# Performance work log

Hardware: AMD Instinct MI355X
Metric: run time of the kernel (lower is better)

The kernel has to match this reference:

```python
import jax, jax.numpy as jnp
import numpy as np
import math

H, HK, D = 16, 4, 128  # n_heads, n_kv_heads, head_dim
WINDOW = 1024
ROPE_BASE = 10000.0
EPS = 1e-6

def _rope_cos_sin(T, dtype):
    inv_freq = 1.0 / (ROPE_BASE ** (jnp.arange(0, D, 2, dtype=jnp.float32) / D))
    ang = jnp.arange(T, dtype=jnp.float32)[:, None] * inv_freq[None, :]  # [T, D/2]
    cos = jnp.concatenate([jnp.cos(ang), jnp.cos(ang)], axis=-1)  # [T, D]
    sin = jnp.concatenate([jnp.sin(ang), jnp.sin(ang)], axis=-1)
    return cos.astype(dtype), sin.astype(dtype)

def _rotate_half(x):
    x1, x2 = jnp.split(x, 2, axis=-1)
    return jnp.concatenate([-x2, x1], axis=-1)

def _apply_rope(t, cos, sin):
    # t: [B, h, T, D]; cos/sin: [T, D]
    return t * cos[None, None] + _rotate_half(t) * sin[None, None]

def setup_inputs() -> dict:
    key = jax.random.key(0)
    ks = jax.random.split(key, 7)
    d = H * D
    s = 1.0 / math.sqrt(d)
    return {
        "x": jax.random.normal(ks[0], (2, 2048, d), jnp.float32),
        "wq": jax.random.normal(ks[1], (H * D, d), jnp.float32) * s,
        "wk": jax.random.normal(ks[2], (HK * D, d), jnp.float32) * s,
        "wv": jax.random.normal(ks[3], (HK * D, d), jnp.float32) * s,
        "wo": jax.random.normal(ks[4], (d, H * D), jnp.float32) * s,
        "gamma_q": jnp.ones((D,), jnp.float32),
        "gamma_k": jnp.ones((D,), jnp.float32),
    }

def reference(x, wq, wk, wv, wo, gamma_q, gamma_k):
    B, T, d = x.shape
    G = H // HK  # query heads per kv head
    # projections (Linear stores [out, in]) -> [B, h, T, D]
    q = jnp.einsum('btd,ed->bte', x, wq).reshape(B, T, H, D).transpose(0, 2, 1, 3)
    k = jnp.einsum('btd,ed->bte', x, wk).reshape(B, T, HK, D).transpose(0, 2, 1, 3)
    v = jnp.einsum('btd,ed->bte', x, wv).reshape(B, T, HK, D).transpose(0, 2, 1, 3)
    cos, sin = _rope_cos_sin(T, x.dtype)
    q = _apply_rope(q, cos, sin)
    k = _apply_rope(k, cos, sin)
    # QK-norm: L2 normalize then learned per-dim scale
    q = q / (jnp.linalg.norm(q, axis=-1, keepdims=True) + EPS) * gamma_q
    k = k / (jnp.linalg.norm(k, axis=-1, keepdims=True) + EPS) * gamma_k
    # GQA: group query heads instead of materializing repeated K/V
    qg = q.reshape(B, HK, G, T, D)
    att = jnp.einsum('bkgtd,bksd->bkgts', qg, k) / math.sqrt(D)  # [B,HK,G,T,T]
    i = jnp.arange(T)
    diff = i[:, None] - i[None, :]
    bad = (diff < 0) | (diff > WINDOW)  # causal OR beyond sliding window
    att = jnp.where(bad[None, None, None], -jnp.inf, att)
    p = jax.nn.softmax(att, axis=-1)
    y = jnp.einsum('bkgts,bksd->bkgtd', p, v)  # [B,HK,G,T,D]
    y = y.reshape(B, H, T, D).transpose(0, 2, 1, 3).reshape(B, T, H * D)
    y = jnp.einsum('bte,de->btd', y, wo)
    return y
```

## Files before the change

### kernel.cpp

```cpp
#include <hip/hip_runtime.h>
#include <cstdint>
#include <cstddef>

typedef unsigned short u16;
typedef short bf16x8 __attribute__((ext_vector_type(8)));
typedef float f32x4 __attribute__((ext_vector_type(4)));

#define MFMA(a,b,c) __builtin_amdgcn_mfma_f32_16x16x32_bf16(a,b,c,0,0,0)

__device__ __forceinline__ u16 f2bf(float f) {
  unsigned u = __builtin_bit_cast(unsigned, f);
  u += 0x7fffu + ((u >> 16) & 1u);
  return (u16)(u >> 16);
}
__device__ __forceinline__ float bf2f(u16 b) {
  return __builtin_bit_cast(float, (unsigned)b << 16);
}
__device__ __forceinline__ float exp2_hw(float x) {
  float r;
  asm("v_exp_f32 %0, %1" : "=v"(r) : "v"(x));
  return r;
}
__device__ __forceinline__ void gl_lds16(const void* g, void* l) {
  __builtin_amdgcn_global_load_lds(
      (const __attribute__((address_space(1))) void*)g,
      (__attribute__((address_space(3))) void*)l, 16, 0, 0);
}
template <int N>
__device__ __forceinline__ void wait_vmcnt() {
  if constexpr (N == 0) asm volatile("s_waitcnt vmcnt(0)" ::: "memory");
  else if constexpr (N == 8) asm volatile("s_waitcnt vmcnt(8)" ::: "memory");
}

__global__ __launch_bounds__(256) void cvt_all(const float* __restrict__ x,
                                               const float* __restrict__ wq,
                                               const float* __restrict__ wk,
                                               const float* __restrict__ wv,
                                               const float* __restrict__ wo,
                                               u16* __restrict__ xb,
                                               u16* __restrict__ wqkvb,
                                               u16* __restrict__ wob) {
  int idx = (blockIdx.x * 256 + threadIdx.x) * 4;
  const float* src;
  u16* dst;
  if (idx < 8388608) { src = x + idx; dst = xb + idx; }
  else if (idx < 12582912) { src = wq + (idx - 8388608); dst = wqkvb + (idx - 8388608); }
  else if (idx < 13631488) { src = wk + (idx - 12582912); dst = wqkvb + (idx - 8388608); }
  else if (idx < 14680064) { src = wv + (idx - 13631488); dst = wqkvb + (idx - 8388608); }
  else if (idx < 18874368) { src = wo + (idx - 14680064); dst = wob + (idx - 14680064); }
  else return;
  float4 v = *(const float4*)src;
  ushort4 o = {f2bf(v.x), f2bf(v.y), f2bf(v.z), f2bf(v.w)};
  *(ushort4*)dst = o;
}

__global__ __launch_bounds__(256) void rope_table(float* __restrict__ ctab,
                                                  float* __restrict__ stab) {
  int i = blockIdx.x * 256 + threadIdx.x;
  int t = i >> 6, f = i & 63;
  float inv_freq = powf(10000.0f, -(2.0f * f) / 128.0f);
  float ang = (float)t * inv_freq;
  ctab[i] = cosf(ang);
  stab[i] = sinf(ang);
}

template <int OUT_F32>
__global__ __launch_bounds__(512, 2) void gemm8p(const u16* __restrict__ A,
                                                 const u16* __restrict__ Bw,
                                                 void* __restrict__ Cout,
                                                 int M, int N, int K) {
  __shared__ u16 As[2][2][128 * 64];
  __shared__ u16 Bs[2][2][128 * 64];
  const int tid = threadIdx.x;
  const int lane = tid & 63;
  const int wv = tid >> 6;
  const int l16 = lane & 15, lhi = lane >> 4;
  const int wm = wv >> 2, wn = wv & 3;
  const int m0 = blockIdx.y * 256;
  const int n0 = blockIdx.x * 256;
  const int nt = K >> 6;

  const int srow8 = lane >> 3;
  const int scol = ((lane & 7) * 16) ^ (srow8 << 4);

  auto stage_tile = [&](int buf, int kt) {
#pragma unroll
    for (int h = 0; h < 2; ++h)
#pragma unroll
      for (int s = 0; s < 2; ++s) {
        int ch = wv + 8 * s;
        int row = m0 + h * 128 + ch * 8 + srow8;
        const char* src = (const char*)A + ((size_t)row * K + (size_t)kt * 64) * 2 + scol;
        gl_lds16(src, (char*)As[buf][h] + ch * 1024);
      }
#pragma unroll
    for (int h = 0; h < 2; ++h)
#pragma unroll
      for (int s = 0; s < 2; ++s) {
        int ch = wv + 8 * s;
        int row = n0 + h * 128 + ch * 8 + srow8;
        const char* src = (const char*)Bw + ((size_t)row * K + (size_t)kt * 64) * 2 + scol;
        gl_lds16(src, (char*)Bs[buf][h] + ch * 1024);
      }
  };
  auto readA = [&](int buf, int mi, int kk) -> bf16x8 {
    int lr = mi * 16 + l16;
    return *(const bf16x8*)((const char*)As[buf][wm] + lr * 128 +
                            ((kk * 64 + lhi * 16) ^ ((l16 & 7) << 4)));
  };
  auto readB = [&](int buf, int ni, int kk) -> bf16x8 {
    int lr = (wn & 1) * 64 + ni * 16 + l16;
    return *(const bf16x8*)((const char*)Bs[buf][wn >> 1] + lr * 128 +
                            ((kk * 64 + lhi * 16) ^ ((l16 & 7) << 4)));
  };

  f32x4 acc[8][4] = {};

  stage_tile(0, 0);
  stage_tile(1, 1);
  wait_vmcnt<8>();
  __builtin_amdgcn_sched_barrier(0);
  __builtin_amdgcn_s_barrier();
  __builtin_amdgcn_sched_barrier(0);

  for (int t = 0; t < nt; ++t) {
    const int b = t & 1;
    bf16x8 bf0[4], af0[8];
#pragma unroll
    for (int ni = 0; ni < 4; ++ni) bf0[ni] = readB(b, ni, 0);
#pragma unroll
    for (int mi = 0; mi < 8; ++mi) af0[mi] = readA(b, mi, 0);
    __builtin_amdgcn_s_setprio(1);
#pragma unroll
    for (int mi = 0; mi < 8; ++mi)
#pragma unroll
      for (int ni = 0; ni < 4; ++ni)
        acc[mi][ni] = MFMA(af0[mi], bf0[ni], acc[mi][ni]);
    __builtin_amdgcn_s_setprio(0);
    bf16x8 bf1[4], af1[8];
#pragma unroll
    for (int ni = 0; ni < 4; ++ni) bf1[ni] = readB(b, ni, 1);
#pragma unroll
    for (int mi = 0; mi < 8; ++mi) af1[mi] = readA(b, mi, 1);
    asm volatile("s_waitcnt lgkmcnt(0)" ::: "memory");
    __builtin_amdgcn_sched_barrier(0);
    __builtin_amdgcn_s_barrier();
    __builtin_amdgcn_sched_barrier(0);
    if (t + 2 < nt) stage_tile(b, t + 2);
    __builtin_amdgcn_s_setprio(1);
#pragma unroll
    for (int mi = 0; mi < 8; ++mi)
#pragma unroll
      for (int ni = 0; ni < 4; ++ni)
        acc[mi][ni] = MFMA(af1[mi], bf1[ni], acc[mi][ni]);
    __builtin_amdgcn_s_setprio(0);
    if (t + 2 < nt) wait_vmcnt<8>();
    else if (t + 1 < nt) wait_vmcnt<0>();
    __builtin_amdgcn_sched_barrier(0);
    __builtin_amdgcn_s_barrier();
    __builtin_amdgcn_sched_barrier(0);
  }

#pragma unroll
  for (int mi = 0; mi < 8; ++mi)
#pragma unroll
    for (int ni = 0; ni < 4; ++ni) {
      int col = n0 + wn * 64 + ni * 16 + l16;
#pragma unroll
      for (int j = 0; j < 4; ++j) {
        int row = m0 + wm * 128 + mi * 16 + lhi * 4 + j;
        float v = acc[mi][ni][j];
        if (OUT_F32)
          ((float*)Cout)[(size_t)row * N + col] = v;
        else
          ((u16*)Cout)[(size_t)row * N + col] = f2bf(v);
      }
    }
}

template <int NH>
__global__ __launch_bounds__(256) void rope_norm(const u16* __restrict__ raw,
                                                 u16* __restrict__ out,
                                                 const float* __restrict__ ctab,
                                                 const float* __restrict__ stab,
                                                 const float* __restrict__ gamma,
                                                 int stride, int coloff, float scale) {
  int gw = blockIdx.x * 4 + (threadIdx.x >> 6);
  int lane = threadIdx.x & 63;
  int h = gw & (NH - 1);
  int bt = gw / NH;
  int t = bt & 2047, bb = bt >> 11;
  const u16* r = raw + (size_t)bt * stride + coloff + (size_t)h * 128;
  ushort2 own = *(const ushort2*)(r + 2 * lane);
  int pk = __shfl_xor(__builtin_bit_cast(int, own), 32);
  ushort2 par = __builtin_bit_cast(ushort2, pk);
  float x0 = bf2f(own.x), x1 = bf2f(own.y);
  float y0 = bf2f(par.x), y1 = bf2f(par.y);
  int f = (lane & 31) * 2;
  float2 c2 = *(const float2*)(ctab + t * 64 + f);
  float2 s2 = *(const float2*)(stab + t * 64 + f);
  bool hi = lane >= 32;
  float e0 = hi ? (x0 * c2.x + y0 * s2.x) : (x0 * c2.x - y0 * s2.x);
  float e1 = hi ? (x1 * c2.y + y1 * s2.y) : (x1 * c2.y - y1 * s2.y);
  float ss = e0 * e0 + e1 * e1;
#pragma unroll
  for (int off = 1; off < 64; off <<= 1) ss += __shfl_xor(ss, off);
  float inv = scale / (sqrtf(ss) + 1e-6f);
  float2 g2 = *(const float2*)(gamma + 2 * lane);
  size_t ob = (((size_t)(bb * NH + h)) * 2048 + t) * 128 + 2 * lane;
  ushort2 o = {f2bf(e0 * inv * g2.x), f2bf(e1 * inv * g2.y)};
  *(ushort2*)(out + ob) = o;
}

__global__ __launch_bounds__(256) void transpose_v(const u16* __restrict__ qkv,
                                                   u16* __restrict__ vt) {
  __shared__ u16 tile[32][33];
  int t0 = blockIdx.x * 32, d0 = blockIdx.y * 32;
  int bh = blockIdx.z;
  int b = bh >> 2, hkk = bh & 3;
  int tx = threadIdx.x & 31, ty = threadIdx.x >> 5;
#pragma unroll
  for (int i = 0; i < 4; ++i) {
    int r = ty + i * 8;
    tile[r][tx] = qkv[((size_t)(b * 2048 + t0 + r)) * 3072 + 2560 + hkk * 128 + d0 + tx];
  }
  __syncthreads();
#pragma unroll
  for (int i = 0; i < 4; ++i) {
    int r = ty + i * 8;
    vt[((size_t)((b * 4 + hkk) * 128 + d0 + r)) * 2048 + t0 + tx] = tile[tx][r];
  }
}

__global__ __launch_bounds__(512, 4) void attn_kernel(const u16* __restrict__ Qr,
                                                      const u16* __restrict__ Kr,
                                                      const u16* __restrict__ Vt,
                                                      u16* __restrict__ Yt) {
  __shared__ u16 Ks[2][64 * 128];
  __shared__ u16 Vs[2][128 * 64];
  __shared__ u16 Ps[8][16 * 64];
  const int tid = threadIdx.x;
  const int lane = tid & 63;
  const int wv = tid >> 6;
  const int l16 = lane & 15, lhi = lane >> 4;
  const int work = (blockIdx.x & 7) * 64 + (blockIdx.x >> 3);
  const int q0b = (work & 15) << 7;
  const int bh = work >> 4;
  const int b = bh >> 4, h = bh & 15;
  const int hk = h >> 2;
  const int q0w = q0b + wv * 16;

  const u16* qbase = Qr + (((size_t)bh) * 2048 + q0w + l16) * 128;
  bf16x8 qf[4];
#pragma unroll
  for (int dc = 0; dc < 4; ++dc)
    qf[dc] = *(const bf16x8*)(qbase + dc * 32 + lhi * 8);

  const char* kg = (const char*)(Kr + ((size_t)(b * 4 + hk)) * 2048 * 128);
  const u16* vg = Vt + ((size_t)(b * 4 + hk)) * 2048 * 128;

  auto stage = [&](int buf, int s0) {
#pragma unroll
    for (int i = 0; i < 2; ++i) {
      int c = wv + 8 * i;
      int row = c * 4 + lhi;
      int srcb = (l16 * 16) ^ ((row & 7) << 4);
      gl_lds16(kg + (size_t)(s0 + row) * 256 + srcb, (char*)Ks[buf] + c * 1024);
    }
    int r8 = lane >> 3, c8 = lane & 7;
#pragma unroll
    for (int i = 0; i < 2; ++i) {
      int c = wv + 8 * i;
      int row = c * 8 + r8;
      int srcb = (c8 * 16) ^ ((r8 & 7) << 4);
      gl_lds16((const char*)(vg + (size_t)row * 2048 + s0) + srcb,
               (char*)Vs[buf] + c * 1024);
    }
  };

  const bf16x8 ones = {0x3F80, 0x3F80, 0x3F80, 0x3F80, 0x3F80, 0x3F80, 0x3F80, 0x3F80};
  float mbase = 0.f;
  f32x4 lacc = {};
  f32x4 oacc[8] = {};

  int s_lo = q0b - 1024; if (s_lo < 0) s_lo = 0;
  const int nt = (q0b + 128 - s_lo) >> 6;

  stage(0, s_lo);
  __syncthreads();
  int cur = 0;
  for (int it = 0; it < nt; ++it) {
    const int s0 = s_lo + (it << 6);
    if (it + 1 < nt) stage(cur ^ 1, s0 + 64);
    const bool skip = (q0w + 15 < s0) || (q0w - (s0 + 63) > 1024);
    if (!skip) {
      f32x4 sacc[4] = {};
      const char* ksb = (const char*)Ks[cur];
      __builtin_amdgcn_s_setprio(1);
#pragma unroll
      for (int n = 0; n < 4; ++n) {
        int row = n * 16 + l16;
#pragma unroll
        for (int dc = 0; dc < 4; ++dc) {
          bf16x8 kf = *(const bf16x8*)(ksb + row * 256 +
                                       ((dc * 64 + lhi * 16) ^ ((l16 & 7) << 4)));
          sacc[n] = MFMA(qf[dc], kf, sacc[n]);
        }
      }
      __builtin_amdgcn_s_setprio(0);
      const bool domask = (q0w < s0 + 63) || (q0w + 15 - s0 > 1024);
      if (domask) {
#pragma unroll
        for (int n = 0; n < 4; ++n)
#pragma unroll
          for (int j = 0; j < 4; ++j) {
            int q = q0w + lhi * 4 + j;
            int s = s0 + n * 16 + l16;
            if ((unsigned)(q - s) > 1024u) sacc[n][j] = -INFINITY;
          }
      }
      float mt = sacc[0][0];
#pragma unroll
      for (int n = 0; n < 4; ++n)
#pragma unroll
        for (int j = 0; j < 4; ++j) mt = fmaxf(mt, sacc[n][j]);
#pragma unroll
      for (int off = 1; off < 64; off <<= 1) mt = fmaxf(mt, __shfl_xor(mt, off));
      if (mt > mbase + 8.f) {
        float sc2 = exp2_hw(mbase - mt);
#pragma unroll
        for (int j = 0; j < 4; ++j) lacc[j] *= sc2;
#pragma unroll
        for (int dt = 0; dt < 8; ++dt)
#pragma unroll
          for (int j = 0; j < 4; ++j) oacc[dt][j] *= sc2;
        mbase = mt;
      }
      char* psb = (char*)Ps[wv];
#pragma unroll
      for (int n = 0; n < 4; ++n)
#pragma unroll
        for (int j = 0; j < 4; ++j) {
          float p = exp2_hw(sacc[n][j] - mbase);
          int R = lhi * 4 + j;
          *(u16*)(psb + R * 128 + (((n * 16 + l16) * 2) ^ ((R & 7) << 4))) = f2bf(p);
        }
      bf16x8 pf[2];
#pragma unroll
      for (int kk = 0; kk < 2; ++kk)
        pf[kk] = *(const bf16x8*)(psb + l16 * 128 +
                                  ((kk * 64 + lhi * 16) ^ ((l16 & 7) << 4)));
      const char* vsb = (const char*)Vs[cur];
      __builtin_amdgcn_s_setprio(1);
      lacc = MFMA(pf[0], ones, lacc);
      lacc = MFMA(pf[1], ones, lacc);
#pragma unroll
      for (int dt = 0; dt < 8; ++dt) {
        int row = dt * 16 + l16;
#pragma unroll
        for (int kk = 0; kk < 2; ++kk) {
          bf16x8 vf = *(const bf16x8*)(vsb + row * 128 +
                                       ((kk * 64 + lhi * 16) ^ ((l16 & 7) << 4)));
          oacc[dt] = MFMA(pf[kk], vf, oacc[dt]);
        }
      }
      __builtin_amdgcn_s_setprio(0);
    }
    __syncthreads();
    cur ^= 1;
  }
#pragma unroll
  for (int j = 0; j < 4; ++j) {
    float inv = 1.0f / lacc[j];
    int q = q0w + lhi * 4 + j;
    size_t rowbase = ((size_t)(b * 2048 + q)) * 2048 + (size_t)h * 128;
#pragma unroll
    for (int dt = 0; dt < 8; ++dt)
      Yt[rowbase + dt * 16 + l16] = f2bf(oacc[dt][j] * inv);
  }
}

extern "C" void kernel_launch(void* const* d_in, const int* in_sizes, int n_in,
                              void* d_out, int out_size, void* d_ws, size_t ws_size,
                              hipStream_t stream) {
  (void)in_sizes; (void)n_in; (void)out_size; (void)ws_size;
  const float* x  = (const float*)d_in[0];
  const float* wq = (const float*)d_in[1];
  const float* wk = (const float*)d_in[2];
  const float* wv = (const float*)d_in[3];
  const float* wo = (const float*)d_in[4];
  const float* gq = (const float*)d_in[5];
  const float* gk = (const float*)d_in[6];
  float* out = (float*)d_out;
  char* ws = (char*)d_ws;

  size_t off = 0;
  auto alloc = [&](size_t bytes) {
    size_t o = off;
    off += (bytes + 255) & ~(size_t)255;
    return o;
  };
  u16* xb     = (u16*)(ws + alloc((size_t)4096 * 2048 * 2));
  u16* wqkvb  = (u16*)(ws + alloc((size_t)3072 * 2048 * 2));
  u16* wob    = (u16*)(ws + alloc((size_t)2048 * 2048 * 2));
  u16* qkvraw = (u16*)(ws + alloc((size_t)4096 * 3072 * 2));
  u16* qr     = (u16*)(ws + alloc((size_t)4096 * 2048 * 2));
  u16* kr     = (u16*)(ws + alloc((size_t)4096 * 512 * 2));
  u16* vt     = (u16*)(ws + alloc((size_t)4096 * 512 * 2));
  float* ctab = (float*)(ws + alloc((size_t)2048 * 64 * 4));
  float* stab = (float*)(ws + alloc((size_t)2048 * 64 * 4));
  u16* ytmp = qkvraw;

  const float sc_log2 = 0.12751744f;

  cvt_all<<<18432, 256, 0, stream>>>(x, wq, wk, wv, wo, xb, wqkvb, wob);
  rope_table<<<512, 256, 0, stream>>>(ctab, stab);

  gemm8p<0><<<dim3(12, 16), 512, 0, stream>>>(xb, wqkvb, qkvraw, 4096, 3072, 2048);

  rope_norm<16><<<16384, 256, 0, stream>>>(qkvraw, qr, ctab, stab, gq, 3072, 0, sc_log2);
  rope_norm<4><<<4096, 256, 0, stream>>>(qkvraw, kr, ctab, stab, gk, 3072, 2048, 1.0f);
  transpose_v<<<dim3(64, 4, 8), 256, 0, stream>>>(qkvraw, vt);

  attn_kernel<<<dim3(512), 512, 0, stream>>>(qr, kr, vt, ytmp);

  gemm8p<1><<<dim3(8, 16), 512, 0, stream>>>(ytmp, wob, out, 4096, 2048, 2048);
}
```

Measured before the change: 211.6 us.

## Templatize GEMM tile shape and use vmcnt-based barriers in attention

```diff
diff --git a/kernel.cpp b/kernel.cpp
--- a/kernel.cpp
+++ b/kernel.cpp
@@ -29,6 +29,8 @@
 template <int N>
 __device__ __forceinline__ void wait_vmcnt() {
   if constexpr (N == 0) asm volatile("s_waitcnt vmcnt(0)" ::: "memory");
+  else if constexpr (N == 4) asm volatile("s_waitcnt vmcnt(4)" ::: "memory");
+  else if constexpr (N == 6) asm volatile("s_waitcnt vmcnt(6)" ::: "memory");
   else if constexpr (N == 8) asm volatile("s_waitcnt vmcnt(8)" ::: "memory");
 }
 
@@ -64,20 +66,27 @@
   stab[i] = sinf(ang);
 }
 
-template <int OUT_F32>
+template <int BM, int BN, int OUT_F32>
 __global__ __launch_bounds__(512, 2) void gemm8p(const u16* __restrict__ A,
                                                  const u16* __restrict__ Bw,
                                                  void* __restrict__ Cout,
                                                  int M, int N, int K) {
-  __shared__ u16 As[2][2][128 * 64];
-  __shared__ u16 Bs[2][2][128 * 64];
+  constexpr int WN = BN / 64;
+  constexpr int WM = 8 / WN;
+  constexpr int MSUB = BM / WM;
+  constexpr int MF = MSUB / 16;
+  constexpr int CHA = BM / 8;
+  constexpr int CPW = (CHA + BN / 8) / 8;
+
+  __shared__ u16 As[2][BM * 64];
+  __shared__ u16 Bs[2][BN * 64];
   const int tid = threadIdx.x;
   const int lane = tid & 63;
   const int wv = tid >> 6;
   const int l16 = lane & 15, lhi = lane >> 4;
-  const int wm = wv >> 2, wn = wv & 3;
-  const int m0 = blockIdx.y * 256;
-  const int n0 = blockIdx.x * 256;
+  const int wm = wv / WN, wn = wv % WN;
+  const int m0 = blockIdx.y * BM;
+  const int n0 = blockIdx.x * BN;
   const int nt = K >> 6;
 
   const int srow8 = lane >> 3;
@@ -85,63 +94,59 @@
 
   auto stage_tile = [&](int buf, int kt) {
 #pragma unroll
-    for (int h = 0; h < 2; ++h)
-#pragma unroll
-      for (int s = 0; s < 2; ++s) {
-        int ch = wv + 8 * s;
-        int row = m0 + h * 128 + ch * 8 + srow8;
+    for (int c = 0; c < CPW; ++c) {
+      int g = wv + 8 * c;
+      if (g < CHA) {
+        int row = m0 + g * 8 + srow8;
         const char* src = (const char*)A + ((size_t)row * K + (size_t)kt * 64) * 2 + scol;
-        gl_lds16(src, (char*)As[buf][h] + ch * 1024);
-      }
-#pragma unroll
-    for (int h = 0; h < 2; ++h)
-#pragma unroll
-      for (int s = 0; s < 2; ++s) {
-        int ch = wv + 8 * s;
-        int row = n0 + h * 128 + ch * 8 + srow8;
+        gl_lds16(src, (char*)As[buf] + g * 1024);
+      } else {
+        int gb = g - CHA;
+        int row = n0 + gb * 8 + srow8;
         const char* src = (const char*)Bw + ((size_t)row * K + (size_t)kt * 64) * 2 + scol;
-        gl_lds16(src, (char*)Bs[buf][h] + ch * 1024);
-      }
+        gl_lds16(src, (char*)Bs[buf] + gb * 1024);
+      }
+    }
   };
   auto readA = [&](int buf, int mi, int kk) -> bf16x8 {
-    int lr = mi * 16 + l16;
-    return *(const bf16x8*)((const char*)As[buf][wm] + lr * 128 +
+    int lr = wm * MSUB + mi * 16 + l16;
+    return *(const bf16x8*)((const char*)As[buf] + lr * 128 +
                             ((kk * 64 + lhi * 16) ^ ((l16 & 7) << 4)));
   };
   auto readB = [&](int buf, int ni, int kk) -> bf16x8 {
-    int lr = (wn & 1) * 64 + ni * 16 + l16;
-    return *(const bf16x8*)((const char*)Bs[buf][wn >> 1] + lr * 128 +
+    int lr = wn * 64 + ni * 16 + l16;
+    return *(const bf16x8*)((const char*)Bs[buf] + lr * 128 +
                             ((kk * 64 + lhi * 16) ^ ((l16 & 7) << 4)));
   };
 
-  f32x4 acc[8][4] = {};
+  f32x4 acc[MF][4] = {};
 
   stage_tile(0, 0);
   stage_tile(1, 1);
-  wait_vmcnt<8>();
+  wait_vmcnt<CPW>();
   __builtin_amdgcn_sched_barrier(0);
   __builtin_amdgcn_s_barrier();
   __builtin_amdgcn_sched_barrier(0);
 
   for (int t = 0; t < nt; ++t) {
     const int b = t & 1;
-    bf16x8 bf0[4], af0[8];
+    bf16x8 bf0[4], af0[MF];
 #pragma unroll
     for (int ni = 0; ni < 4; ++ni) bf0[ni] = readB(b, ni, 0);
 #pragma unroll
-    for (int mi = 0; mi < 8; ++mi) af0[mi] = readA(b, mi, 0);
+    for (int mi = 0; mi < MF; ++mi) af0[mi] = readA(b, mi, 0);
     __builtin_amdgcn_s_setprio(1);
 #pragma unroll
-    for (int mi = 0; mi < 8; ++mi)
+    for (int mi = 0; mi < MF; ++mi)
 #pragma unroll
       for (int ni = 0; ni < 4; ++ni)
         acc[mi][ni] = MFMA(af0[mi], bf0[ni], acc[mi][ni]);
     __builtin_amdgcn_s_setprio(0);
-    bf16x8 bf1[4], af1[8];
+    bf16x8 bf1[4], af1[MF];
 #pragma unroll
     for (int ni = 0; ni < 4; ++ni) bf1[ni] = readB(b, ni, 1);
 #pragma unroll
-    for (int mi = 0; mi < 8; ++mi) af1[mi] = readA(b, mi, 1);
+    for (int mi = 0; mi < MF; ++mi) af1[mi] = readA(b, mi, 1);
     asm volatile("s_waitcnt lgkmcnt(0)" ::: "memory");
     __builtin_amdgcn_sched_barrier(0);
     __builtin_amdgcn_s_barrier();
@@ -149,12 +154,12 @@
     if (t + 2 < nt) stage_tile(b, t + 2);
     __builtin_amdgcn_s_setprio(1);
 #pragma unroll
-    for (int mi = 0; mi < 8; ++mi)
+    for (int mi = 0; mi < MF; ++mi)
 #pragma unroll
       for (int ni = 0; ni < 4; ++ni)
         acc[mi][ni] = MFMA(af1[mi], bf1[ni], acc[mi][ni]);
     __builtin_amdgcn_s_setprio(0);
-    if (t + 2 < nt) wait_vmcnt<8>();
+    if (t + 2 < nt) wait_vmcnt<CPW>();
     else if (t + 1 < nt) wait_vmcnt<0>();
     __builtin_amdgcn_sched_barrier(0);
     __builtin_amdgcn_s_barrier();
@@ -162,13 +167,13 @@
   }
 
 #pragma unroll
-  for (int mi = 0; mi < 8; ++mi)
+  for (int mi = 0; mi < MF; ++mi)
 #pragma unroll
     for (int ni = 0; ni < 4; ++ni) {
       int col = n0 + wn * 64 + ni * 16 + l16;
 #pragma unroll
       for (int j = 0; j < 4; ++j) {
-        int row = m0 + wm * 128 + mi * 16 + lhi * 4 + j;
+        int row = m0 + wm * MSUB + mi * 16 + lhi * 4 + j;
         float v = acc[mi][ni][j];
         if (OUT_F32)
           ((float*)Cout)[(size_t)row * N + col] = v;
@@ -287,11 +292,18 @@
   const int nt = (q0b + 128 - s_lo) >> 6;
 
   stage(0, s_lo);
-  __syncthreads();
   int cur = 0;
   for (int it = 0; it < nt; ++it) {
     const int s0 = s_lo + (it << 6);
-    if (it + 1 < nt) stage(cur ^ 1, s0 + 64);
+    if (it + 1 < nt) {
+      stage(cur ^ 1, s0 + 64);
+      wait_vmcnt<4>();
+    } else {
+      wait_vmcnt<0>();
+    }
+    __builtin_amdgcn_sched_barrier(0);
+    __builtin_amdgcn_s_barrier();
+    __builtin_amdgcn_sched_barrier(0);
     const bool skip = (q0w + 15 < s0) || (q0w - (s0 + 63) > 1024);
     if (!skip) {
       f32x4 sacc[4] = {};
@@ -366,7 +378,9 @@
       }
       __builtin_amdgcn_s_setprio(0);
     }
-    __syncthreads();
+    __builtin_amdgcn_sched_barrier(0);
+    __builtin_amdgcn_s_barrier();
+    __builtin_amdgcn_sched_barrier(0);
     cur ^= 1;
   }
 #pragma unroll
@@ -416,7 +430,7 @@
   cvt_all<<<18432, 256, 0, stream>>>(x, wq, wk, wv, wo, xb, wqkvb, wob);
   rope_table<<<512, 256, 0, stream>>>(ctab, stab);
 
-  gemm8p<0><<<dim3(12, 16), 512, 0, stream>>>(xb, wqkvb, qkvraw, 4096, 3072, 2048);
+  gemm8p<256, 256, 0><<<dim3(12, 16), 512, 0, stream>>>(xb, wqkvb, qkvraw, 4096, 3072, 2048);
 
   rope_norm<16><<<16384, 256, 0, stream>>>(qkvraw, qr, ctab, stab, gq, 3072, 0, sc_log2);
   rope_norm<4><<<4096, 256, 0, stream>>>(qkvraw, kr, ctab, stab, gk, 3072, 2048, 1.0f);
@@ -424,5 +438,5 @@
 
   attn_kernel<<<dim3(512), 512, 0, stream>>>(qr, kr, vt, ytmp);
 
-  gemm8p<1><<<dim3(8, 16), 512, 0, stream>>>(ytmp, wob, out, 4096, 2048, 2048);
-}
+  gemm8p<256, 128, 1><<<dim3(16, 16), 512, 0, stream>>>(ytmp, wob, out, 4096, 2048, 2048);
+}
```

New measurement: 198.4 us. 1.07x faster.

## Restructure GEMM pipelines with quarter-staged loads and retile output projection

Applied to the files above, without the earlier changes.

```diff
diff --git a/kernel.cpp b/kernel.cpp
--- a/kernel.cpp
+++ b/kernel.cpp
@@ -29,7 +29,19 @@
 template <int N>
 __device__ __forceinline__ void wait_vmcnt() {
   if constexpr (N == 0) asm volatile("s_waitcnt vmcnt(0)" ::: "memory");
+  else if constexpr (N == 2) asm volatile("s_waitcnt vmcnt(2)" ::: "memory");
+  else if constexpr (N == 4) asm volatile("s_waitcnt vmcnt(4)" ::: "memory");
+  else if constexpr (N == 6) asm volatile("s_waitcnt vmcnt(6)" ::: "memory");
   else if constexpr (N == 8) asm volatile("s_waitcnt vmcnt(8)" ::: "memory");
+}
+__device__ __forceinline__ void lgkm0_fence() {
+  asm volatile("s_waitcnt lgkmcnt(0)" ::: "memory");
+  __builtin_amdgcn_sched_barrier(0);
+}
+__device__ __forceinline__ void block_barrier() {
+  __builtin_amdgcn_sched_barrier(0);
+  __builtin_amdgcn_s_barrier();
+  __builtin_amdgcn_sched_barrier(0);
 }
 
 __global__ __launch_bounds__(256) void cvt_all(const float* __restrict__ x,
@@ -64,13 +76,12 @@
   stab[i] = sinf(ang);
 }
 
-template <int OUT_F32>
-__global__ __launch_bounds__(512, 2) void gemm8p(const u16* __restrict__ A,
+__global__ __launch_bounds__(512, 2) void gemm_q(const u16* __restrict__ A,
                                                  const u16* __restrict__ Bw,
-                                                 void* __restrict__ Cout,
+                                                 u16* __restrict__ Cout,
                                                  int M, int N, int K) {
-  __shared__ u16 As[2][2][128 * 64];
-  __shared__ u16 Bs[2][2][128 * 64];
+  __shared__ u16 As[2][256 * 64];
+  __shared__ u16 Bs[2][256 * 64];
   const int tid = threadIdx.x;
   const int lane = tid & 63;
   const int wv = tid >> 6;
@@ -83,82 +94,90 @@
   const int srow8 = lane >> 3;
   const int scol = ((lane & 7) * 16) ^ (srow8 << 4);
 
-  auto stage_tile = [&](int buf, int kt) {
-#pragma unroll
-    for (int h = 0; h < 2; ++h)
-#pragma unroll
-      for (int s = 0; s < 2; ++s) {
-        int ch = wv + 8 * s;
-        int row = m0 + h * 128 + ch * 8 + srow8;
-        const char* src = (const char*)A + ((size_t)row * K + (size_t)kt * 64) * 2 + scol;
-        gl_lds16(src, (char*)As[buf][h] + ch * 1024);
-      }
-#pragma unroll
-    for (int h = 0; h < 2; ++h)
-#pragma unroll
-      for (int s = 0; s < 2; ++s) {
-        int ch = wv + 8 * s;
-        int row = n0 + h * 128 + ch * 8 + srow8;
-        const char* src = (const char*)Bw + ((size_t)row * K + (size_t)kt * 64) * 2 + scol;
-        gl_lds16(src, (char*)Bs[buf][h] + ch * 1024);
-      }
-  };
-  auto readA = [&](int buf, int mi, int kk) -> bf16x8 {
-    int lr = mi * 16 + l16;
-    return *(const bf16x8*)((const char*)As[buf][wm] + lr * 128 +
+  auto stA = [&](int buf, int kt, int g) {
+    int row = m0 + g * 8 + srow8;
+    const char* src = (const char*)A + ((size_t)row * K + (size_t)kt * 64) * 2 + scol;
+    gl_lds16(src, (char*)As[buf] + g * 1024);
+  };
+  auto stB = [&](int buf, int kt, int g) {
+    int row = n0 + g * 8 + srow8;
+    const char* src = (const char*)Bw + ((size_t)row * K + (size_t)kt * 64) * 2 + scol;
+    gl_lds16(src, (char*)Bs[buf] + g * 1024);
+  };
+  auto rdA = [&](int buf, int mi, int kk) -> bf16x8 {
+    int row = wm * 128 + mi * 16 + l16;
+    return *(const bf16x8*)((const char*)As[buf] + row * 128 +
                             ((kk * 64 + lhi * 16) ^ ((l16 & 7) << 4)));
   };
-  auto readB = [&](int buf, int ni, int kk) -> bf16x8 {
-    int lr = (wn & 1) * 64 + ni * 16 + l16;
-    return *(const bf16x8*)((const char*)Bs[buf][wn >> 1] + lr * 128 +
+  auto rdB = [&](int buf, int ni, int kk) -> bf16x8 {
+    int row = wn * 64 + ni * 16 + l16;
+    return *(const bf16x8*)((const char*)Bs[buf] + row * 128 +
                             ((kk * 64 + lhi * 16) ^ ((l16 & 7) << 4)));
   };
 
   f32x4 acc[8][4] = {};
 
-  stage_tile(0, 0);
-  stage_tile(1, 1);
-  wait_vmcnt<8>();
-  __builtin_amdgcn_sched_barrier(0);
-  __builtin_amdgcn_s_barrier();
-  __builtin_amdgcn_sched_barrier(0);
+  stB(0, 0, wv); stB(0, 0, wv + 8); stB(0, 0, wv + 16); stB(0, 0, wv + 24);
+  stA(0, 0, wv); stA(0, 0, wv + 16); stA(0, 0, wv + 8); stA(0, 0, wv + 24);
+  stB(1, 1, wv); stB(1, 1, wv + 8);
+  stB(1, 1, wv + 16); stB(1, 1, wv + 24);
+  stA(1, 1, wv); stA(1, 1, wv + 16);
+  stA(1, 1, wv + 8); stA(1, 1, wv + 24);
 
   for (int t = 0; t < nt; ++t) {
-    const int b = t & 1;
-    bf16x8 bf0[4], af0[8];
-#pragma unroll
-    for (int ni = 0; ni < 4; ++ni) bf0[ni] = readB(b, ni, 0);
-#pragma unroll
-    for (int mi = 0; mi < 8; ++mi) af0[mi] = readA(b, mi, 0);
+    const int b = t & 1, ob = b ^ 1;
+    const bool st = (t >= 1) && (t + 1 < nt);
+    const bool last = (t == nt - 1);
+    bf16x8 bf[2][4], af[2][2];
+
+    if (st) { stB(ob, t + 1, wv); stB(ob, t + 1, wv + 8); }
+    if (last) wait_vmcnt<2>(); else if (t == 0) wait_vmcnt<8>(); else wait_vmcnt<4>();
+    block_barrier();
+#pragma unroll
+    for (int kk = 0; kk < 2; ++kk)
+#pragma unroll
+      for (int ni = 0; ni < 4; ++ni) bf[kk][ni] = rdB(b, ni, kk);
+#pragma unroll
+    for (int kk = 0; kk < 2; ++kk) { af[0][kk] = rdA(b, 0, kk); af[1][kk] = rdA(b, 1, kk); }
+    lgkm0_fence();
     __builtin_amdgcn_s_setprio(1);
 #pragma unroll
-    for (int mi = 0; mi < 8; ++mi)
-#pragma unroll
-      for (int ni = 0; ni < 4; ++ni)
-        acc[mi][ni] = MFMA(af0[mi], bf0[ni], acc[mi][ni]);
+    for (int mi = 0; mi < 2; ++mi)
+#pragma unroll
+      for (int kk = 0; kk < 2; ++kk)
+#pragma unroll
+        for (int ni = 0; ni < 4; ++ni)
+          acc[mi][ni] = MFMA(af[mi][kk], bf[kk][ni], acc[mi][ni]);
     __builtin_amdgcn_s_setprio(0);
-    bf16x8 bf1[4], af1[8];
-#pragma unroll
-    for (int ni = 0; ni < 4; ++ni) bf1[ni] = readB(b, ni, 1);
-#pragma unroll
-    for (int mi = 0; mi < 8; ++mi) af1[mi] = readA(b, mi, 1);
-    asm volatile("s_waitcnt lgkmcnt(0)" ::: "memory");
-    __builtin_amdgcn_sched_barrier(0);
-    __builtin_amdgcn_s_barrier();
-    __builtin_amdgcn_sched_barrier(0);
-    if (t + 2 < nt) stage_tile(b, t + 2);
-    __builtin_amdgcn_s_setprio(1);
-#pragma unroll
-    for (int mi = 0; mi < 8; ++mi)
-#pragma unroll
-      for (int ni = 0; ni < 4; ++ni)
-        acc[mi][ni] = MFMA(af1[mi], bf1[ni], acc[mi][ni]);
-    __builtin_amdgcn_s_setprio(0);
-    if (t + 2 < nt) wait_vmcnt<8>();
-    else if (t + 1 < nt) wait_vmcnt<0>();
-    __builtin_amdgcn_sched_barrier(0);
-    __builtin_amdgcn_s_barrier();
-    __builtin_amdgcn_sched_barrier(0);
+
+#pragma unroll
+    for (int q = 1; q < 4; ++q) {
+      if (st) {
+        if (q == 1) { stB(ob, t + 1, wv + 16); stB(ob, t + 1, wv + 24); }
+        else if (q == 2) { stA(ob, t + 1, wv); stA(ob, t + 1, wv + 16); }
+        else { stA(ob, t + 1, wv + 8); stA(ob, t + 1, wv + 24); }
+      }
+      if (last) { if (q < 2) wait_vmcnt<2>(); else wait_vmcnt<0>(); }
+      else if (t == 0) wait_vmcnt<8>();
+      else wait_vmcnt<4>();
+      block_barrier();
+#pragma unroll
+      for (int kk = 0; kk < 2; ++kk) {
+        af[0][kk] = rdA(b, 2 * q, kk);
+        af[1][kk] = rdA(b, 2 * q + 1, kk);
+      }
+      lgkm0_fence();
+      __builtin_amdgcn_s_setprio(1);
+#pragma unroll
+      for (int mi = 0; mi < 2; ++mi)
+#pragma unroll
+        for (int kk = 0; kk < 2; ++kk)
+#pragma unroll
+          for (int ni = 0; ni < 4; ++ni)
+            acc[2 * q + mi][ni] = MFMA(af[mi][kk], bf[kk][ni], acc[2 * q + mi][ni]);
+      __builtin_amdgcn_s_setprio(0);
+    }
+    block_barrier();
   }
 
 #pragma unroll
@@ -169,11 +188,115 @@
 #pragma unroll
       for (int j = 0; j < 4; ++j) {
         int row = m0 + wm * 128 + mi * 16 + lhi * 4 + j;
-        float v = acc[mi][ni][j];
-        if (OUT_F32)
-          ((float*)Cout)[(size_t)row * N + col] = v;
-        else
-          ((u16*)Cout)[(size_t)row * N + col] = f2bf(v);
+        Cout[(size_t)row * N + col] = f2bf(acc[mi][ni][j]);
+      }
+    }
+}
+
+__global__ __launch_bounds__(512, 2) void gemm_o(const u16* __restrict__ A,
+                                                 const u16* __restrict__ Bw,
+                                                 float* __restrict__ Cout,
+                                                 int M, int N, int K) {
+  __shared__ u16 As[2][256 * 64];
+  __shared__ u16 Bs[2][128 * 64];
+  const int tid = threadIdx.x;
+  const int lane = tid & 63;
+  const int wv = tid >> 6;
+  const int l16 = lane & 15, lhi = lane >> 4;
+  const int wm = wv >> 1, wn = wv & 1;
+  const int m0 = blockIdx.y * 256;
+  const int n0 = blockIdx.x * 128;
+  const int nt = K >> 6;
+
+  const int srow8 = lane >> 3;
+  const int scol = ((lane & 7) * 16) ^ (srow8 << 4);
+
+  auto stA = [&](int buf, int kt, int g) {
+    int row = m0 + g * 8 + srow8;
+    const char* src = (const char*)A + ((size_t)row * K + (size_t)kt * 64) * 2 + scol;
+    gl_lds16(src, (char*)As[buf] + g * 1024);
+  };
+  auto stB = [&](int buf, int kt, int g) {
+    int row = n0 + g * 8 + srow8;
+    const char* src = (const char*)Bw + ((size_t)row * K + (size_t)kt * 64) * 2 + scol;
+    gl_lds16(src, (char*)Bs[buf] + g * 1024);
+  };
+  auto rdA = [&](int buf, int mi, int kk) -> bf16x8 {
+    int row = wm * 64 + mi * 16 + l16;
+    return *(const bf16x8*)((const char*)As[buf] + row * 128 +
+                            ((kk * 64 + lhi * 16) ^ ((l16 & 7) << 4)));
+  };
+  auto rdB = [&](int buf, int ni, int kk) -> bf16x8 {
+    int row = wn * 64 + ni * 16 + l16;
+    return *(const bf16x8*)((const char*)Bs[buf] + row * 128 +
+                            ((kk * 64 + lhi * 16) ^ ((l16 & 7) << 4)));
+  };
+
+  const int c0a = (wv & 3) + (wv >> 2) * 8;
+  const int c0b = c0a + 16;
+  const int c1a = c0a + 4;
+  const int c1b = c0a + 20;
+
+  f32x4 acc[4][4] = {};
+
+  stB(0, 0, wv); stB(0, 0, wv + 8); stA(0, 0, c0a); stA(0, 0, c0b);
+  stA(0, 0, c1a); stA(0, 0, c1b);
+  stB(1, 1, wv); stB(1, 1, wv + 8); stA(1, 1, c0a); stA(1, 1, c0b);
+  stA(1, 1, c1a); stA(1, 1, c1b);
+
+  for (int t = 0; t < nt; ++t) {
+    const int b = t & 1, ob = b ^ 1;
+    const bool st = (t >= 1) && (t + 1 < nt);
+    const bool last = (t == nt - 1);
+    bf16x8 bf[2][4], af[2][2];
+
+    if (st) { stB(ob, t + 1, wv); stB(ob, t + 1, wv + 8); stA(ob, t + 1, c0a); stA(ob, t + 1, c0b); }
+    if (last) wait_vmcnt<2>(); else wait_vmcnt<6>();
+    block_barrier();
+#pragma unroll
+    for (int kk = 0; kk < 2; ++kk)
+#pragma unroll
+      for (int ni = 0; ni < 4; ++ni) bf[kk][ni] = rdB(b, ni, kk);
+#pragma unroll
+    for (int kk = 0; kk < 2; ++kk) { af[0][kk] = rdA(b, 0, kk); af[1][kk] = rdA(b, 1, kk); }
+    lgkm0_fence();
+    __builtin_amdgcn_s_setprio(1);
+#pragma unroll
+    for (int mi = 0; mi < 2; ++mi)
+#pragma unroll
+      for (int kk = 0; kk < 2; ++kk)
+#pragma unroll
+        for (int ni = 0; ni < 4; ++ni)
+          acc[mi][ni] = MFMA(af[mi][kk], bf[kk][ni], acc[mi][ni]);
+    __builtin_amdgcn_s_setprio(0);
+
+    if (st) { stA(ob, t + 1, c1a); stA(ob, t + 1, c1b); }
+    if (last) wait_vmcnt<0>(); else wait_vmcnt<6>();
+    block_barrier();
+#pragma unroll
+    for (int kk = 0; kk < 2; ++kk) { af[0][kk] = rdA(b, 2, kk); af[1][kk] = rdA(b, 3, kk); }
+    lgkm0_fence();
+    __builtin_amdgcn_s_setprio(1);
+#pragma unroll
+    for (int mi = 0; mi < 2; ++mi)
+#pragma unroll
+      for (int kk = 0; kk < 2; ++kk)
+#pragma unroll
+        for (int ni = 0; ni < 4; ++ni)
+          acc[2 + mi][ni] = MFMA(af[mi][kk], bf[kk][ni], acc[2 + mi][ni]);
+    __builtin_amdgcn_s_setprio(0);
+    block_barrier();
+  }
+
+#pragma unroll
+  for (int mi = 0; mi < 4; ++mi)
+#pragma unroll
+    for (int ni = 0; ni < 4; ++ni) {
+      int col = n0 + wn * 64 + ni * 16 + l16;
+#pragma unroll
+      for (int j = 0; j < 4; ++j) {
+        int row = m0 + wm * 64 + mi * 16 + lhi * 4 + j;
+        Cout[(size_t)row * N + col] = acc[mi][ni][j];
       }
     }
 }
@@ -287,11 +410,16 @@
   const int nt = (q0b + 128 - s_lo) >> 6;
 
   stage(0, s_lo);
-  __syncthreads();
   int cur = 0;
   for (int it = 0; it < nt; ++it) {
     const int s0 = s_lo + (it << 6);
-    if (it + 1 < nt) stage(cur ^ 1, s0 + 64);
+    if (it + 1 < nt) {
+      stage(cur ^ 1, s0 + 64);
+      wait_vmcnt<4>();
+    } else {
+      wait_vmcnt<0>();
+    }
+    block_barrier();
     const bool skip = (q0w + 15 < s0) || (q0w - (s0 + 63) > 1024);
     if (!skip) {
       f32x4 sacc[4] = {};
@@ -366,7 +494,7 @@
       }
       __builtin_amdgcn_s_setprio(0);
     }
-    __syncthreads();
+    block_barrier();
     cur ^= 1;
   }
 #pragma unroll
@@ -416,7 +544,7 @@
   cvt_all<<<18432, 256, 0, stream>>>(x, wq, wk, wv, wo, xb, wqkvb, wob);
   rope_table<<<512, 256, 0, stream>>>(ctab, stab);
 
-  gemm8p<0><<<dim3(12, 16), 512, 0, stream>>>(xb, wqkvb, qkvraw, 4096, 3072, 2048);
+  gemm_q<<<dim3(12, 16), 512, 0, stream>>>(xb, wqkvb, qkvraw, 4096, 3072, 2048);
 
   rope_norm<16><<<16384, 256, 0, stream>>>(qkvraw, qr, ctab, stab, gq, 3072, 0, sc_log2);
   rope_norm<4><<<4096, 256, 0, stream>>>(qkvraw, kr, ctab, stab, gk, 3072, 2048, 1.0f);
@@ -424,5 +552,5 @@
 
   attn_kernel<<<dim3(512), 512, 0, stream>>>(qr, kr, vt, ytmp);
 
-  gemm8p<1><<<dim3(8, 16), 512, 0, stream>>>(ytmp, wob, out, 4096, 2048, 2048);
-}
+  gemm_o<<<dim3(16, 16), 512, 0, stream>>>(ytmp, wob, out, 4096, 2048, 2048);
+}
```

New measurement: 311.1 us. +47.0%, slower.
